# Optimization experiments

Measured on AMD Instinct MI355X. Metric: run time of the kernel, lower is better.

Reference implementation:

```python
import jax, jax.numpy as jnp
import numpy as np

MLP_DIMS = [256, 128, 64, 32, 1]

def setup_inputs() -> dict:
    key = jax.random.key(0)
    ks = jax.random.split(key, 16)
    N, C, sp = 2, 256, 512
    inp = {
        'points': jax.random.normal(ks[0], (N, C, sp), dtype=jnp.float32),
        'heatMap': jax.random.uniform(ks[1], (N, sp, sp), dtype=jnp.float32),
        'mask': jnp.ones((N, sp, sp), dtype=jnp.float32),
        'positiveMask': jax.random.uniform(ks[2], (N, sp, sp), dtype=jnp.float32),
    }
    # MLP params: 256->128->64->32->1, Kaiming-ish scale
    for i, (din, dout) in enumerate(zip(MLP_DIMS[:-1], MLP_DIMS[1:])):
        inp[f'W{i}'] = jax.random.normal(ks[4 + i], (din, dout), dtype=jnp.float32) * (1.0 / np.sqrt(din))
        inp[f'b{i}'] = jnp.zeros((dout,), dtype=jnp.float32)
    return inp


def _mlp(x, Ws, bs):
    # Linear+ReLU cascade; final layer is a raw logit (no activation).
    n = len(Ws)
    for i, (W, b) in enumerate(zip(Ws, bs)):
        x = jnp.einsum('...i,io->...o', x, W) + b
        if i < n - 1:
            x = jax.nn.relu(x)
    return x


def _bce_with_logits(logits, targets):
    # stable elementwise BCE-with-logits, reduction='none'
    return jnp.maximum(logits, 0.0) - logits * targets + jnp.log1p(jnp.exp(-jnp.abs(logits)))


def reference(points, heatMap, mask, positiveMask, W0, b0, W1, b1, W2, b2, W3, b3):
    p = jnp.transpose(points, (0, 2, 1))          # (N, sp, C)
    X = p[:, :, None, :] + p[:, None, :, :]       # (N, sp, sp, C)
    pred = _mlp(X, [W0, W1, W2, W3], [b0, b1, b2, b3])[..., 0]  # (N, sp, sp)
    loss = _bce_with_logits(pred, heatMap) * mask * positiveMask
    loss = loss.sum() / positiveMask.sum()
    return (pred, loss)
```

## Files before the change

### kernel.cpp

```cpp
#include <hip/hip_runtime.h>
#include <hip/hip_bf16.h>
#include <stdint.h>

#define N_ 2
#define C_ 256
#define SP 512
#define H1 128
#define H2 64
#define H3 32
#define NTILE 1056
#define GRID 256

using f32x4 = __attribute__((ext_vector_type(4))) float;
using u32x4 = __attribute__((ext_vector_type(4))) unsigned int;
using s16x8 = __attribute__((ext_vector_type(8))) short;

__device__ __forceinline__ uint32_t f2bf_rne(float x) {
    uint32_t u = __builtin_bit_cast(uint32_t, x);
    return (u + 0x7FFFu + ((u >> 16) & 1u)) >> 16;
}
__device__ __forceinline__ float bf2f(uint32_t h) {
    return __builtin_bit_cast(float, h << 16);
}
__device__ __forceinline__ uint32_t pkbf(float a, float b) {
    __hip_bfloat162 h = __float22bfloat162_rn(make_float2(a, b));
    uint32_t r;
    __builtin_memcpy(&r, &h, 4);
    return r;
}
__device__ __forceinline__ uint16_t bf1(float a) {
    __hip_bfloat16 h = __float2bfloat16(a);
    uint16_t r;
    __builtin_memcpy(&r, &h, 2);
    return r;
}
__device__ __forceinline__ f32x4 ntload4(const float* p) {
    return __builtin_nontemporal_load((const f32x4*)p);
}

__device__ __forceinline__ void unrank_tile(int tau, int& n, int& iBase, int& jBase)
{
    int nn = (tau >= 528) ? 1 : 0;
    int u = tau - nn * 528;
    int bi = (int)((65.0f - sqrtf(4225.0f - 8.0f * (float)u)) * 0.5f);
    int s = bi * (65 - bi) / 2;
    while (s > u) { --bi; s = bi * (65 - bi) / 2; }
    while (u - s >= 32 - bi) { ++bi; s = bi * (65 - bi) / 2; }
    int bj = bi + (u - s);
    n = nn; iBase = bi * 16; jBase = bj * 16;
}

__global__ __launch_bounds__(512) void k_precompA(
    const float* __restrict__ points, const float* __restrict__ W0,
    const float* __restrict__ b0,
    const float* __restrict__ W1, const float* __restrict__ W2,
    float* __restrict__ A,
    short* __restrict__ W1Th, short* __restrict__ W2Th, short* __restrict__ W2Tl,
    float* __restrict__ accum)
{
    int t = threadIdx.x;
    if (blockIdx.x == 0 && t < 4) accum[t] = 0.0f;
    int k4 = t & 31;
    int team = t >> 5;
    int rloc = team & 3, cq = team >> 2;
    int row = blockIdx.x * 4 + rloc;
    int n = row >> 9, i = row & (SP - 1);
    const float* pb = points + (size_t)n * C_ * SP + i;
    f32x4 p0 = {0.f, 0.f, 0.f, 0.f}, p1 = {0.f, 0.f, 0.f, 0.f};
    int c0 = cq * 64;
#pragma unroll 8
    for (int c = c0; c < c0 + 64; c += 2) {
        float s0 = pb[(size_t)c * SP];
        float s1 = pb[(size_t)(c + 1) * SP];
        f32x4 w0v = *(const f32x4*)(W0 + c * H1 + k4 * 4);
        f32x4 w1v = *(const f32x4*)(W0 + (c + 1) * H1 + k4 * 4);
#pragma unroll
        for (int e = 0; e < 4; ++e) {
            p0[e] = fmaf(s0, w0v[e], p0[e]);
            p1[e] = fmaf(s1, w1v[e], p1[e]);
        }
    }
#pragma unroll
    for (int e = 0; e < 4; ++e) p0[e] += p1[e];
    __shared__ f32x4 part[16][32];
    part[team][k4] = p0;
    __syncthreads();
    int r2 = t >> 7, kk = t & 127;
    float s = 0.5f * b0[kk]
            + part[r2][kk >> 2][kk & 3] + part[r2 + 4][kk >> 2][kk & 3]
            + part[r2 + 8][kk >> 2][kk & 3] + part[r2 + 12][kk >> 2][kk & 3];
    A[(size_t)(blockIdx.x * 4 + r2) * H1 + kk] = s;

    int gid = blockIdx.x * 512 + t;
    int gstride = gridDim.x * 512;
    for (int idx = gid; idx < H2 * H1; idx += gstride) {
        int col = idx >> 7, k = idx & 127;
        int sidx = col * 128 + ((((k >> 3) ^ (col & 15)) << 3) | (k & 7));
        W1Th[sidx] = (short)f2bf_rne(W1[k * H2 + col]);
    }
    for (int idx = gid; idx < H3 * H2; idx += gstride) {
        int col = idx >> 6, k = idx & 63;
        float wv = W2[k * H3 + col];
        uint32_t h = f2bf_rne(wv);
        int sidx = col * 64 + ((((k >> 3) ^ (col & 7)) << 3) | (k & 7));
        W2Th[sidx] = (short)h;
        W2Tl[sidx] = (short)f2bf_rne(wv - bf2f(h));
    }
}

__global__ __launch_bounds__(512, 2) void k_main(
    const float* __restrict__ A,
    const short* __restrict__ wtab,
    const float* __restrict__ b1, const float* __restrict__ b2,
    const float* __restrict__ W3, const float* __restrict__ b3,
    const float* __restrict__ heat, const float* __restrict__ mask,
    const float* __restrict__ pos,
    float* __restrict__ pred, float* __restrict__ accum, float* __restrict__ loss)
{
    __shared__ __align__(16) char smem[32768 + 16384 + 8192 + 2176 + 64];
    int t = threadIdx.x;
    int bid = blockIdx.x;
    int l = t & 63, w = t >> 6;
    int lc = l & 15, kg = l >> 4;
    char* x2 = smem + 32768 + w * 2048;
    char* x3 = smem + 32768 + 16384 + w * 1024;
    char* zbB = smem + 32768 + 16384 + 8192;
    float* rb = (float*)(smem + 32768 + 16384 + 8192 + 2176);

    const short* lw1h = wtab;
    const short* lw2h = wtab + 8192;
    const short* lw2l = wtab + 10240;

    int rST = t >> 5, segST = t & 31;

    s16x8 bw3;
    {
        f32x4 wa = *(const f32x4*)(W3 + kg * 8);
        f32x4 wb = *(const f32x4*)(W3 + kg * 8 + 4);
        u32x4 wp;
        wp[0] = pkbf(wa[0], wa[1]);
        wp[1] = pkbf(wa[2], wa[3]);
        wp[2] = pkbf(wb[0], wb[1]);
        wp[3] = pkbf(wb[2], wb[3]);
        bw3 = __builtin_bit_cast(s16x8, wp);
    }
    float b3v = b3[0];

    float num = 0.0f, den = 0.0f;

    {
        int n0, ib0, jb0; unrank_tile(bid, n0, ib0, jb0);
        const float* Ab = A + (size_t)n0 * SP * H1;
        f32x4 va = ntload4(Ab + (size_t)(ib0 + rST) * H1 + segST * 4);
        f32x4 vb = ntload4(Ab + (size_t)(jb0 + rST) * H1 + segST * 4);
        *(f32x4*)(smem + rST * 512 + ((segST ^ rST) << 4)) = va;
        *(f32x4*)(smem + 8192 + rST * 512 + ((segST ^ rST) << 4)) = vb;
    }
    __syncthreads();

    int cur = 0, itp = 0;
    for (int tau = bid; tau < NTILE; tau += GRID, cur ^= 1, itp ^= 1) {
        int n, iBase, jBase; unrank_tile(tau, n, iBase, jBase);
        char* aiA = smem + cur * 16384;
        char* ajA = aiA + 8192;
        float* zb = (float*)(zbB + itp * 1088);

        bool hn = (tau + GRID < NTILE);
        f32x4 sva, svb;
        if (hn) {
            int n1, ib1, jb1; unrank_tile(tau + GRID, n1, ib1, jb1);
            const float* Ab1 = A + (size_t)n1 * SP * H1;
            sva = ntload4(Ab1 + (size_t)(ib1 + rST) * H1 + segST * 4);
            svb = ntload4(Ab1 + (size_t)(jb1 + rST) * H1 + segST * 4);
        }

        int pr = (t & 255) >> 4, pc = t & 15;
        size_t idx_e = (t < 256)
            ? ((size_t)n * SP + iBase + pr) * SP + (jBase + pc)
            : ((size_t)n * SP + jBase + pr) * SP + (iBase + pc);
        float tg_e = __builtin_nontemporal_load(heat + idx_e);
        float mk_e = __builtin_nontemporal_load(mask + idx_e);
        float pm_e = __builtin_nontemporal_load(pos + idx_e);

        f32x4 acc[2][4];
#pragma unroll
        for (int cf = 0; cf < 4; ++cf) {
            float bv = b1[cf * 16 + lc];
            acc[0][cf] = (f32x4){bv, bv, bv, bv};
            acc[1][cf] = (f32x4){bv, bv, bv, bv};
        }
#pragma unroll
        for (int ks = 0; ks < 4; ++ks) {
            int g0 = ks * 8 + kg * 2;
            f32x4 aj0 = *(const f32x4*)(ajA + lc * 512 + ((g0 ^ lc) << 4));
            f32x4 aj1 = *(const f32x4*)(ajA + lc * 512 + (((g0 + 1) ^ lc) << 4));
#pragma unroll
            for (int m = 0; m < 2; ++m) {
                int rl = 2 * w + m;
                f32x4 ai0 = *(const f32x4*)(aiA + rl * 512 + ((g0 ^ rl) << 4));
                f32x4 ai1 = *(const f32x4*)(aiA + rl * 512 + (((g0 + 1) ^ rl) << 4));
                float xs[8];
#pragma unroll
                for (int e = 0; e < 4; ++e) {
                    xs[e]     = fmaxf(ai0[e] + aj0[e], 0.0f);
                    xs[4 + e] = fmaxf(ai1[e] + aj1[e], 0.0f);
                }
                u32x4 hw;
#pragma unroll
                for (int p = 0; p < 4; ++p)
                    hw[p] = pkbf(xs[2 * p], xs[2 * p + 1]);
                s16x8 ahi = __builtin_bit_cast(s16x8, hw);
#pragma unroll
                for (int cf = 0; cf < 4; ++cf) {
                    int boff = (cf * 16 + lc) * 128 + (((ks * 4 + kg) ^ lc) << 3);
                    s16x8 bhi = *(const s16x8*)(lw1h + boff);
                    acc[m][cf] = __builtin_amdgcn_mfma_f32_16x16x32_bf16(ahi, bhi, acc[m][cf], 0, 0, 0);
                }
            }
        }

#pragma unroll
        for (int m = 0; m < 2; ++m) {
#pragma unroll
            for (int cf = 0; cf < 4; ++cf) {
                int g = cf * 2 + (lc >> 3);
#pragma unroll
                for (int r = 0; r < 4; ++r) {
                    int row = kg * 4 + r;
                    int off = row * 128 + ((g ^ (row & 7)) << 4) + (lc & 7) * 2;
                    *(uint16_t*)(x2 + off) = bf1(fmaxf(acc[m][cf][r], 0.0f));
                }
            }
            f32x4 acc2[2];
#pragma unroll
            for (int cf = 0; cf < 2; ++cf) {
                float bv = b2[cf * 16 + lc];
                acc2[cf] = (f32x4){bv, bv, bv, bv};
            }
#pragma unroll
            for (int ks = 0; ks < 2; ++ks) {
                int aoff = lc * 128 + (((ks * 4 + kg) ^ (lc & 7)) << 4);
                s16x8 xa = *(const s16x8*)(x2 + aoff);
#pragma unroll
                for (int cf = 0; cf < 2; ++cf) {
                    int b2off = (cf * 16 + lc) * 64 + (((ks * 4 + kg) ^ (lc & 7)) << 3);
                    s16x8 bh = *(const s16x8*)(lw2h + b2off);
                    s16x8 bl = *(const s16x8*)(lw2l + b2off);
                    acc2[cf] = __builtin_amdgcn_mfma_f32_16x16x32_bf16(xa, bh, acc2[cf], 0, 0, 0);
                    acc2[cf] = __builtin_amdgcn_mfma_f32_16x16x32_bf16(xa, bl, acc2[cf], 0, 0, 0);
                }
            }
#pragma unroll
            for (int cf = 0; cf < 2; ++cf) {
                int g = cf * 2 + (lc >> 3);
#pragma unroll
                for (int r = 0; r < 4; ++r) {
                    int row = kg * 4 + r;
                    int off = row * 64 + ((g ^ (row & 3)) << 4) + (lc & 7) * 2;
                    *(uint16_t*)(x3 + off) = bf1(fmaxf(acc2[cf][r], 0.0f));
                }
            }
            int a4off = lc * 64 + ((kg ^ (lc & 3)) << 4);
            s16x8 x4 = *(const s16x8*)(x3 + a4off);
            f32x4 acc3 = (f32x4){b3v, b3v, b3v, b3v};
            acc3 = __builtin_amdgcn_mfma_f32_16x16x32_bf16(x4, bw3, acc3, 0, 0, 0);
            if (lc == 0) {
#pragma unroll
                for (int r = 0; r < 4; ++r)
                    zb[(2 * w + m) * 17 + kg * 4 + r] = acc3[r];
            }
        }

        if (hn) {
            char* Aalt = smem + (cur ^ 1) * 16384;
            *(f32x4*)(Aalt + rST * 512 + ((segST ^ rST) << 4)) = sva;
            *(f32x4*)(Aalt + 8192 + rST * 512 + ((segST ^ rST) << 4)) = svb;
        }
        __syncthreads();

        if (t < 256) {
            int i = iBase + pr, j = jBase + pc;
            if (j >= i) {
                float z = zb[pr * 17 + pc];
                __builtin_nontemporal_store(z, pred + idx_e);
                float bce = fmaxf(z, 0.0f) - z * tg_e + __logf(1.0f + __expf(-fabsf(z)));
                num += bce * mk_e * pm_e;
                den += pm_e;
            }
        } else {
            int J = jBase + pr, I = iBase + pc;
            if (J > I) {
                float z = zb[pc * 17 + pr];
                __builtin_nontemporal_store(z, pred + idx_e);
                float bce = fmaxf(z, 0.0f) - z * tg_e + __logf(1.0f + __expf(-fabsf(z)));
                num += bce * mk_e * pm_e;
                den += pm_e;
            }
        }
    }

#pragma unroll
    for (int off = 32; off > 0; off >>= 1) {
        num += __shfl_down(num, off, 64);
        den += __shfl_down(den, off, 64);
    }
    if (l == 0) { rb[w] = num; rb[8 + w] = den; }
    __syncthreads();
    if (t == 0) {
        float sn = 0.0f, sd = 0.0f;
#pragma unroll
        for (int q = 0; q < 8; ++q) { sn += rb[q]; sd += rb[8 + q]; }
        atomicAdd(&accum[0], sn);
        atomicAdd(&accum[1], sd);
        __threadfence();
        unsigned done = atomicAdd((unsigned*)&accum[2], 1u);
        if (done == GRID - 1) {
            float fn = atomicAdd(&accum[0], 0.0f);
            float fd = atomicAdd(&accum[1], 0.0f);
            loss[0] = fn / fd;
        }
    }
}

extern "C" void kernel_launch(void* const* d_in, const int* in_sizes, int n_in,
                              void* d_out, int out_size, void* d_ws, size_t ws_size,
                              hipStream_t stream)
{
    const float* points = (const float*)d_in[0];
    const float* heat   = (const float*)d_in[1];
    const float* mask   = (const float*)d_in[2];
    const float* pos    = (const float*)d_in[3];
    const float* W0     = (const float*)d_in[4];
    const float* b0     = (const float*)d_in[5];
    const float* W1     = (const float*)d_in[6];
    const float* b1     = (const float*)d_in[7];
    const float* W2     = (const float*)d_in[8];
    const float* b2     = (const float*)d_in[9];
    const float* W3     = (const float*)d_in[10];
    const float* b3     = (const float*)d_in[11];

    float* pred = (float*)d_out;
    float* loss = pred + (size_t)N_ * SP * SP;

    char* ws = (char*)d_ws;
    float* accum = (float*)ws;
    float* A     = (float*)(ws + 256);
    short* W1Th  = (short*)(ws + 256 + 524288);
    short* W2Th  = (short*)(ws + 256 + 524288 + 16384);
    short* W2Tl  = (short*)(ws + 256 + 524288 + 20480);

    k_precompA<<<256, 512, 0, stream>>>(points, W0, b0, W1, W2, A,
                                        W1Th, W2Th, W2Tl, accum);
    k_main<<<GRID, 512, 0, stream>>>(
        A, W1Th, b1, b2, W3, b3, heat, mask, pos, pred, accum, loss);
}
```

Before: 40.42 us.

## Fuse precompute and main kernels into one cooperative kernel with grid sync

Merges the precompute kernel (first-layer projection A, transposed bf16 weight tables, accumulator reset) into the main kernel and launches it cooperatively, with a grid-wide barrier between the two phases. The aim is to remove the second kernel launch and the gap between the two kernels. In exchange it adds a grid sync, requires all 256 blocks to be co-resident, and moves the prologue under the main kernel's launch bounds, where it shares shared memory.

```diff
diff --git a/kernel.cpp b/kernel.cpp
--- a/kernel.cpp
+++ b/kernel.cpp
@@ -1,6 +1,9 @@
 #include <hip/hip_runtime.h>
 #include <hip/hip_bf16.h>
+#include <hip/hip_cooperative_groups.h>
 #include <stdint.h>
+
+namespace cg = cooperative_groups;
 
 #define N_ 2
 #define C_ 256
@@ -50,76 +53,73 @@
     n = nn; iBase = bi * 16; jBase = bj * 16;
 }
 
-__global__ __launch_bounds__(512) void k_precompA(
+__global__ __launch_bounds__(512, 2) void k_fused(
     const float* __restrict__ points, const float* __restrict__ W0,
     const float* __restrict__ b0,
     const float* __restrict__ W1, const float* __restrict__ W2,
-    float* __restrict__ A,
-    short* __restrict__ W1Th, short* __restrict__ W2Th, short* __restrict__ W2Tl,
-    float* __restrict__ accum)
-{
-    int t = threadIdx.x;
-    if (blockIdx.x == 0 && t < 4) accum[t] = 0.0f;
-    int k4 = t & 31;
-    int team = t >> 5;
-    int rloc = team & 3, cq = team >> 2;
-    int row = blockIdx.x * 4 + rloc;
-    int n = row >> 9, i = row & (SP - 1);
-    const float* pb = points + (size_t)n * C_ * SP + i;
-    f32x4 p0 = {0.f, 0.f, 0.f, 0.f}, p1 = {0.f, 0.f, 0.f, 0.f};
-    int c0 = cq * 64;
-#pragma unroll 8
-    for (int c = c0; c < c0 + 64; c += 2) {
-        float s0 = pb[(size_t)c * SP];
-        float s1 = pb[(size_t)(c + 1) * SP];
-        f32x4 w0v = *(const f32x4*)(W0 + c * H1 + k4 * 4);
-        f32x4 w1v = *(const f32x4*)(W0 + (c + 1) * H1 + k4 * 4);
-#pragma unroll
-        for (int e = 0; e < 4; ++e) {
-            p0[e] = fmaf(s0, w0v[e], p0[e]);
-            p1[e] = fmaf(s1, w1v[e], p1[e]);
-        }
-    }
-#pragma unroll
-    for (int e = 0; e < 4; ++e) p0[e] += p1[e];
-    __shared__ f32x4 part[16][32];
-    part[team][k4] = p0;
-    __syncthreads();
-    int r2 = t >> 7, kk = t & 127;
-    float s = 0.5f * b0[kk]
-            + part[r2][kk >> 2][kk & 3] + part[r2 + 4][kk >> 2][kk & 3]
-            + part[r2 + 8][kk >> 2][kk & 3] + part[r2 + 12][kk >> 2][kk & 3];
-    A[(size_t)(blockIdx.x * 4 + r2) * H1 + kk] = s;
-
-    int gid = blockIdx.x * 512 + t;
-    int gstride = gridDim.x * 512;
-    for (int idx = gid; idx < H2 * H1; idx += gstride) {
-        int col = idx >> 7, k = idx & 127;
-        int sidx = col * 128 + ((((k >> 3) ^ (col & 15)) << 3) | (k & 7));
-        W1Th[sidx] = (short)f2bf_rne(W1[k * H2 + col]);
-    }
-    for (int idx = gid; idx < H3 * H2; idx += gstride) {
-        int col = idx >> 6, k = idx & 63;
-        float wv = W2[k * H3 + col];
-        uint32_t h = f2bf_rne(wv);
-        int sidx = col * 64 + ((((k >> 3) ^ (col & 7)) << 3) | (k & 7));
-        W2Th[sidx] = (short)h;
-        W2Tl[sidx] = (short)f2bf_rne(wv - bf2f(h));
-    }
-}
-
-__global__ __launch_bounds__(512, 2) void k_main(
-    const float* __restrict__ A,
-    const short* __restrict__ wtab,
     const float* __restrict__ b1, const float* __restrict__ b2,
     const float* __restrict__ W3, const float* __restrict__ b3,
     const float* __restrict__ heat, const float* __restrict__ mask,
     const float* __restrict__ pos,
+    float* __restrict__ A,
+    short* __restrict__ W1Th, short* __restrict__ W2Th, short* __restrict__ W2Tl,
     float* __restrict__ pred, float* __restrict__ accum, float* __restrict__ loss)
 {
     __shared__ __align__(16) char smem[32768 + 16384 + 8192 + 2176 + 64];
     int t = threadIdx.x;
     int bid = blockIdx.x;
+
+    {
+        if (bid == 0 && t < 4) accum[t] = 0.0f;
+        int k4 = t & 31;
+        int team = t >> 5;
+        int rloc = team & 3, cq = team >> 2;
+        int row = bid * 4 + rloc;
+        int n = row >> 9, i = row & (SP - 1);
+        const float* pb = points + (size_t)n * C_ * SP + i;
+        f32x4 p0 = {0.f, 0.f, 0.f, 0.f}, p1 = {0.f, 0.f, 0.f, 0.f};
+        int c0 = cq * 64;
+#pragma unroll 8
+        for (int c = c0; c < c0 + 64; c += 2) {
+            float s0 = pb[(size_t)c * SP];
+            float s1 = pb[(size_t)(c + 1) * SP];
+            f32x4 w0v = *(const f32x4*)(W0 + c * H1 + k4 * 4);
+            f32x4 w1v = *(const f32x4*)(W0 + (c + 1) * H1 + k4 * 4);
+#pragma unroll
+            for (int e = 0; e < 4; ++e) {
+                p0[e] = fmaf(s0, w0v[e], p0[e]);
+                p1[e] = fmaf(s1, w1v[e], p1[e]);
+            }
+        }
+#pragma unroll
+        for (int e = 0; e < 4; ++e) p0[e] += p1[e];
+        f32x4* part = (f32x4*)smem;
+        part[team * 32 + k4] = p0;
+        __syncthreads();
+        int r2 = t >> 7, kk = t & 127;
+        float s = 0.5f * b0[kk]
+                + part[r2 * 32 + (kk >> 2)][kk & 3] + part[(r2 + 4) * 32 + (kk >> 2)][kk & 3]
+                + part[(r2 + 8) * 32 + (kk >> 2)][kk & 3] + part[(r2 + 12) * 32 + (kk >> 2)][kk & 3];
+        A[(size_t)(bid * 4 + r2) * H1 + kk] = s;
+
+        int gid = bid * 512 + t;
+        int gstride = GRID * 512;
+        for (int idx = gid; idx < H2 * H1; idx += gstride) {
+            int col = idx >> 7, k = idx & 127;
+            int sidx = col * 128 + ((((k >> 3) ^ (col & 15)) << 3) | (k & 7));
+            W1Th[sidx] = (short)f2bf_rne(W1[k * H2 + col]);
+        }
+        for (int idx = gid; idx < H3 * H2; idx += gstride) {
+            int col = idx >> 6, k = idx & 63;
+            float wv = W2[k * H3 + col];
+            uint32_t h = f2bf_rne(wv);
+            int sidx = col * 64 + ((((k >> 3) ^ (col & 7)) << 3) | (k & 7));
+            W2Th[sidx] = (short)h;
+            W2Tl[sidx] = (short)f2bf_rne(wv - bf2f(h));
+        }
+    }
+    cg::this_grid().sync();
+
     int l = t & 63, w = t >> 6;
     int lc = l & 15, kg = l >> 4;
     char* x2 = smem + 32768 + w * 2048;
@@ -127,9 +127,9 @@
     char* zbB = smem + 32768 + 16384 + 8192;
     float* rb = (float*)(smem + 32768 + 16384 + 8192 + 2176);
 
-    const short* lw1h = wtab;
-    const short* lw2h = wtab + 8192;
-    const short* lw2l = wtab + 10240;
+    const short* lw1h = W1Th;
+    const short* lw2h = W2Th;
+    const short* lw2l = W2Tl;
 
     int rST = t >> 5, segST = t & 31;
 
@@ -349,8 +349,13 @@
     short* W2Th  = (short*)(ws + 256 + 524288 + 16384);
     short* W2Tl  = (short*)(ws + 256 + 524288 + 20480);
 
-    k_precompA<<<256, 512, 0, stream>>>(points, W0, b0, W1, W2, A,
-                                        W1Th, W2Th, W2Tl, accum);
-    k_main<<<GRID, 512, 0, stream>>>(
-        A, W1Th, b1, b2, W3, b3, heat, mask, pos, pred, accum, loss);
-}
+    void* args[] = {
+        (void*)&points, (void*)&W0, (void*)&b0, (void*)&W1, (void*)&W2,
+        (void*)&b1, (void*)&b2, (void*)&W3, (void*)&b3,
+        (void*)&heat, (void*)&mask, (void*)&pos,
+        (void*)&A, (void*)&W1Th, (void*)&W2Th, (void*)&W2Tl,
+        (void*)&pred, (void*)&accum, (void*)&loss
+    };
+    hipLaunchCooperativeKernel((void*)k_fused, dim3(GRID), dim3(512),
+                               args, 0, stream);
+}
```

Result: slower. 80.37 us (+98.8%).
